# Optimization experiments

Measured on AMD Instinct MI355X. Metric: run time of the kernel, lower is better.

Reference implementation:

```python
import jax, jax.numpy as jnp
import numpy as np

KS = 3
PAD = 1
N = KS * KS  # 9 sampling taps


def conv2d(x, w, b=None):
    out = jax.lax.conv_general_dilated(
        x, w, window_strides=(1, 1), padding=((PAD, PAD), (PAD, PAD)),
        dimension_numbers=('NCHW', 'OIHW', 'NCHW'))
    if b is not None:
        out = out + b[None, :, None, None]
    return out


def deform_conv(x, w_p, b_p, w_m, b_m, w_c):
    """Modulated deformable conv (DCNv2, pure-python reference style)."""
    b, c, h, w = x.shape
    offset = conv2d(x, w_p, b_p)               # [b, 2N, h, w]
    m = jax.nn.sigmoid(conv2d(x, w_m, b_m))    # [b, N, h, w]
    xp = jnp.pad(x, ((0, 0), (0, 0), (PAD, PAD), (PAD, PAD)))
    hp, wp = h + 2 * PAD, w + 2 * PAD
    # kernel-relative offsets p_n and base grid p_0 (coords in padded image)
    r = jnp.arange(-(KS - 1) // 2, (KS - 1) // 2 + 1, dtype=x.dtype)
    pn_x, pn_y = jnp.meshgrid(r, r, indexing='ij')
    pn = jnp.concatenate([pn_x.reshape(-1), pn_y.reshape(-1)])  # [2N]
    p0_x, p0_y = jnp.meshgrid(jnp.arange(1, h + 1, dtype=x.dtype),
                              jnp.arange(1, w + 1, dtype=x.dtype), indexing='ij')
    p0 = jnp.concatenate([jnp.tile(p0_x[None], (N, 1, 1)),
                          jnp.tile(p0_y[None], (N, 1, 1))])     # [2N, h, w]
    p = jnp.transpose(offset + p0[None] + pn[None, :, None, None], (0, 2, 3, 1))  # [b,h,w,2N]
    px, py = p[..., :N], p[..., N:]
    fx, fy = jnp.floor(px), jnp.floor(py)
    q_lt_x = jnp.clip(fx, 0, hp - 1)
    q_lt_y = jnp.clip(fy, 0, wp - 1)
    q_rb_x = jnp.clip(fx + 1, 0, hp - 1)
    q_rb_y = jnp.clip(fy + 1, 0, wp - 1)
    px = jnp.clip(px, 0, hp - 1)
    py = jnp.clip(py, 0, wp - 1)
    # bilinear weights for the 4 integer corners
    g_lt = (1 + (q_lt_x - px)) * (1 + (q_lt_y - py))
    g_rb = (1 - (q_rb_x - px)) * (1 - (q_rb_y - py))
    g_lb = (1 + (q_lt_x - px)) * (1 - (q_rb_y - py))
    g_rt = (1 - (q_rb_x - px)) * (1 + (q_lt_y - py))
    xf = xp.reshape(b, c, hp * wp)

    def gather(qx, qy):
        idx = (qx * wp + qy).astype(jnp.int32).reshape(b, 1, h * w * N)
        idx = jnp.broadcast_to(idx, (b, c, h * w * N))
        return jnp.take_along_axis(xf, idx, axis=2).reshape(b, c, h, w, N)

    x_off = (g_lt[:, None] * gather(q_lt_x, q_lt_y)
             + g_rb[:, None] * gather(q_rb_x, q_rb_y)
             + g_lb[:, None] * gather(q_lt_x, q_rb_y)
             + g_rt[:, None] * gather(q_rb_x, q_lt_y))   # [b,c,h,w,N]
    x_off = x_off * jnp.transpose(m, (0, 2, 3, 1))[:, None]  # modulation
    # Conv2d(kernel=ks, stride=ks) over the reshaped taps == einsum over (c, n)
    return jnp.einsum('bchwn,ocn->bohw', x_off, w_c.reshape(w_c.shape[0], c, N))


def setup_inputs() -> dict:
    key = jax.random.key(0)
    ks = jax.random.split(key, 12)
    b, dim, hid, H, W = 8, 256, 1024, 28, 28
    inp = {
        'x': jax.random.normal(ks[0], (b, dim, H, W), jnp.float32),
        'w_p1': jax.random.normal(ks[1], (2 * N, dim, KS, KS), jnp.float32) * 0.01,
        'b_p1': jnp.zeros((2 * N,), jnp.float32),
        'w_m1': jax.random.normal(ks[2], (N, dim, KS, KS), jnp.float32) * 0.05,
        'b_m1': jnp.zeros((N,), jnp.float32),
        'w_c1': jax.random.normal(ks[3], (hid, dim, KS, KS), jnp.float32) * 0.02,
        'w_p2': jax.random.normal(ks[4], (2 * N, hid, KS, KS), jnp.float32) * 0.01,
        'b_p2': jnp.zeros((2 * N,), jnp.float32),
        'w_m2': jax.random.normal(ks[5], (N, hid, KS, KS), jnp.float32) * 0.05,
        'b_m2': jnp.zeros((N,), jnp.float32),
        'w_c2': jax.random.normal(ks[6], (dim, hid, KS, KS), jnp.float32) * 0.01,
    }
    return inp


def reference(x, w_p1, b_p1, w_m1, b_m1, w_c1, w_p2, b_p2, w_m2, b_m2, w_c2):
    h = jax.nn.relu(deform_conv(x, w_p1, b_p1, w_m1, b_m1, w_c1))
    # dropout p=0.0 -> identity (eval)
    return deform_conv(h, w_p2, b_p2, w_m2, b_m2, w_c2)
```

## Files before the change

### kernel.cpp

```cpp
#include <hip/hip_runtime.h>
#include <hip/hip_bf16.h>
#include <math.h>

#define B 8
#define HH 28
#define WDIM 28
#define PIX 784
#define PPIX 900
#define M_TOT 6272
#define NK 9
#define C1 256
#define HID 1024
#define OUT2 256
#define K1 (C1*9)
#define NY 2560
#define KSP1 12

typedef short short8_t __attribute__((ext_vector_type(8)));
typedef unsigned short us8 __attribute__((ext_vector_type(8)));
typedef unsigned short us4 __attribute__((ext_vector_type(4)));
typedef float f32x4 __attribute__((ext_vector_type(4)));

__device__ inline float bf2f(unsigned short u){ union{unsigned i; float f;} w; w.i=((unsigned)u)<<16; return w.f; }
__device__ inline unsigned short f2bf(float f){ union{float ff; unsigned i;} w; w.ff=f; unsigned u=w.i; return (unsigned short)((u + 0x7FFFu + ((u>>16)&1u))>>16); }

__device__ inline void gload16(const void* g, void* l) {
  __builtin_amdgcn_global_load_lds((const __attribute__((address_space(1))) void*)g,
                                   (__attribute__((address_space(3))) void*)l, 16, 0, 0);
}

__device__ inline int xcd_swz(int bid, int nwg) {
  int q = nwg >> 3, r = nwg & 7;
  int xcd = bid & 7, idx = bid >> 3;
  int base = (xcd < r) ? xcd * (q + 1) : r * (q + 1) + (xcd - r) * q;
  return base + idx;
}

__global__ __launch_bounds__(256) void ring_zero2(
    unsigned short* __restrict__ xclp, unsigned short* __restrict__ Y)
{
  int bid = blockIdx.x;
  unsigned short* buf; int C;
  if (bid < B * 116) { buf = xclp; C = C1; }
  else               { buf = Y; C = NY; bid -= B * 116; }
  int r = bid % 116, b = bid / 116;
  int h, w;
  if (r < 30)      { h = 0;  w = r; }
  else if (r < 60) { h = 29; w = r - 30; }
  else if (r < 88) { h = r - 59; w = 0; }
  else             { h = r - 87; w = 29; }
  unsigned short* row = buf + ((size_t)b * PPIX + h * 30 + w) * C;
  for (int c = threadIdx.x * 8; c < C; c += 2048)
    *(us8*)(row + c) = us8{0,0,0,0,0,0,0,0};
}

__global__ __launch_bounds__(256) void xpose_kernel(
    const float* __restrict__ x, unsigned short* __restrict__ xclp, int C)
{
  __shared__ unsigned short tile[32][33];
  int b = blockIdx.z, c0 = blockIdx.y * 32, p0 = blockIdx.x * 32;
  int tx = threadIdx.x & 31, ty = threadIdx.x >> 5;
  for (int i = ty; i < 32; i += 8) {
    int c = c0 + i, p = p0 + tx;
    unsigned short v = 0;
    if (p < PIX) v = f2bf(x[((size_t)b * C + c) * PIX + p]);
    tile[i][tx] = v;
  }
  __syncthreads();
  for (int i = ty; i < 32; i += 8) {
    int p = p0 + i, c = c0 + tx;
    if (p < PIX) {
      int h = p / WDIM, w = p % WDIM;
      xclp[((size_t)b * PPIX + (h + 1) * 30 + (w + 1)) * C + c] = tile[tx][i];
    }
  }
}

__global__ __launch_bounds__(256) void wprep_all(
    const float* __restrict__ wc1, const float* __restrict__ wp1,
    const float* __restrict__ wm1, const float* __restrict__ wc2,
    const float* __restrict__ wp2, const float* __restrict__ wm2,
    unsigned short* __restrict__ wr1, unsigned short* __restrict__ wpr1,
    unsigned short* __restrict__ wy2)
{
  __shared__ float lds[HID * 9];
  int bid = blockIdx.x;
  if (bid < HID) {
    for (int i = threadIdx.x; i < K1; i += 256) lds[i] = wc1[(size_t)bid * K1 + i];
    __syncthreads();
    for (int k = threadIdx.x; k < K1; k += 256) {
      int n = k >> 8, c = k & 255;
      wr1[(size_t)bid * K1 + k] = f2bf(lds[c * 9 + n]);
    }
    return;
  }
  if (bid < HID + 32) {
    int ch = bid - HID;
    const float* src = nullptr;
    if (ch < 18) src = wp1 + (size_t)ch * K1;
    else if (ch < 27) src = wm1 + (size_t)(ch - 18) * K1;
    for (int i = threadIdx.x; i < K1; i += 256) lds[i] = src ? src[i] : 0.f;
    __syncthreads();
    for (int k = threadIdx.x; k < K1; k += 256) {
      int n = k >> 8, c = k & 255;
      wpr1[(size_t)ch * K1 + k] = f2bf(lds[c * 9 + n]);
    }
    return;
  }
  bid -= HID + 32;
  if (bid >= 283) {
    int j = 2547 + (bid - 283);
    for (int c = threadIdx.x; c < HID; c += 256) wy2[(size_t)j * HID + c] = 0;
    return;
  }
  const float* src;
  if (bid < 256) src = wc2 + (size_t)bid * HID * 9;
  else {
    int ch = bid - 256;
    src = (ch < 18) ? wp2 + (size_t)ch * HID * 9 : wm2 + (size_t)(ch - 18) * HID * 9;
  }
  for (int i = threadIdx.x; i < HID * 9; i += 256) lds[i] = src[i];
  __syncthreads();
  #pragma unroll
  for (int n = 0; n < 9; ++n) {
    int j = (bid < 256) ? n * 256 + bid : 2304 + n * 27 + (bid - 256);
    for (int c = threadIdx.x; c < HID; c += 256)
      wy2[(size_t)j * HID + c] = f2bf(lds[c * 9 + n]);
  }
}

template<int C, int KSPLIT>
__global__ __launch_bounds__(256) void pconv_mfma(
    const unsigned short* __restrict__ xclp,
    const unsigned short* __restrict__ wpr,
    float* __restrict__ pmpart)
{
  __shared__ unsigned short As[2][128 * 64];
  __shared__ unsigned short Ws[2][32 * 64];
  const int K = 9 * C;
  int t = threadIdx.x, lane = t & 63, wv = t >> 6;
  int m0 = blockIdx.x * 128;
  int kz = blockIdx.y;
  int wm = (wv & 1) * 64, wo = (wv >> 1) * 16;
  f32x4 acc[4];
  #pragma unroll
  for (int i = 0; i < 4; ++i) acc[i] = {0.f, 0.f, 0.f, 0.f};
  long pbase[4];
  #pragma unroll
  for (int i = 0; i < 4; ++i) {
    int L = i * 256 + t, row = L >> 3;
    int m = m0 + row, b = m / PIX, pix = m - b * PIX;
    int h = pix / WDIM, w = pix - h * WDIM;
    pbase[i] = ((long)b * PPIX + (h + 1) * 30 + (w + 1)) * C;
  }
  auto stage = [&](int buf, int kk) {
    int n = kk / C, c0 = kk - n * C;
    long doff = (long)(((n / 3) - 1) * 30 + (n % 3) - 1) * C + c0;
    #pragma unroll
    for (int i = 0; i < 4; ++i) {
      int L = i * 256 + t, row = L >> 3, ch = L & 7;
      const char* src = (const char*)(xclp + pbase[i] + doff) + ((ch ^ (row & 7)) << 4);
      gload16(src, (char*)As[buf] + (size_t)(i * 256 + (wv << 6)) * 16);
    }
    {
      int row = t >> 3, ch = t & 7;
      const char* src = (const char*)(wpr + (size_t)row * K + kk) + ((ch ^ (row & 7)) << 4);
      gload16(src, (char*)Ws[buf] + (size_t)(wv << 6) * 16);
    }
  };

  int kbeg = kz * (K / KSPLIT), kend = kbeg + K / KSPLIT;
  stage(0, kbeg);
  asm volatile("s_waitcnt vmcnt(0)" ::: "memory");
  __syncthreads();
  int cur = 0;
  for (int k0 = kbeg; k0 < kend; k0 += 64, cur ^= 1) {
    if (k0 + 64 < kend) stage(cur ^ 1, k0 + 64);
    #pragma unroll
    for (int ks = 0; ks < 2; ++ks) {
      short8_t af[4], bq;
      {
        int row = wo + (lane & 15), ch = ks * 4 + (lane >> 4);
        bq = *(const short8_t*)((const char*)Ws[cur] + row * 128 + ((ch ^ (row & 7)) << 4));
      }
      #pragma unroll
      for (int fm = 0; fm < 4; ++fm) {
        int row = wm + fm * 16 + (lane & 15), ch = ks * 4 + (lane >> 4);
        af[fm] = *(const short8_t*)((const char*)As[cur] + row * 128 + ((ch ^ (row & 7)) << 4));
      }
      #pragma unroll
      for (int fm = 0; fm < 4; ++fm)
        acc[fm] = __builtin_amdgcn_mfma_f32_16x16x32_bf16(af[fm], bq, acc[fm], 0, 0, 0);
    }
    asm volatile("s_waitcnt vmcnt(0)" ::: "memory");
    __syncthreads();
  }
  float* dst = pmpart + (size_t)kz * M_TOT * 32;
  #pragma unroll
  for (int fm = 0; fm < 4; ++fm)
    #pragma unroll
    for (int r = 0; r < 4; ++r) {
      int ml = m0 + wm + fm * 16 + (lane >> 4) * 4 + r;
      int o = wo + (lane & 15);
      dst[(size_t)ml * 32 + o] = acc[fm][r];
    }
}

__device__ inline void mktab_emit(int m, int n, float ox, float oy, float om,
                                  const float* b_p, const float* b_m,
                                  int4* tabOff, float4* tabG)
{
  int bidx = m / PIX, pix = m % PIX;
  int hh = pix / WDIM, ww = pix % WDIM;
  float px = ox + b_p[n]     + (float)(hh + 1) + (float)(n / 3 - 1);
  float py = oy + b_p[9 + n] + (float)(ww + 1) + (float)(n % 3 - 1);
  float msk = 1.f / (1.f + expf(-(om + b_m[n])));
  float fx = floorf(px), fy = floorf(py);
  float qlx = fminf(fmaxf(fx, 0.f), 29.f);
  float qly = fminf(fmaxf(fy, 0.f), 29.f);
  float qrx = fminf(fmaxf(fx + 1.f, 0.f), 29.f);
  float qry = fminf(fmaxf(fy + 1.f, 0.f), 29.f);
  float pxc = fminf(fmaxf(px, 0.f), 29.f);
  float pyc = fminf(fmaxf(py, 0.f), 29.f);
  float glt = (1.f + (qlx - pxc)) * (1.f + (qly - pyc));
  float grb = (1.f - (qrx - pxc)) * (1.f - (qry - pyc));
  float glb = (1.f + (qlx - pxc)) * (1.f - (qry - pyc));
  float grt = (1.f - (qrx - pxc)) * (1.f + (qly - pyc));
  int ax = (int)qlx, ay = (int)qly, bx = (int)qrx, by = (int)qry;
  int pb = bidx * PPIX;
  *tabOff = make_int4(pb + ax * 30 + ay, pb + bx * 30 + by,
                      pb + ax * 30 + by, pb + bx * 30 + ay);
  *tabG   = make_float4(glt * msk, grb * msk, glb * msk, grt * msk);
}

template<int CIN, int KSPLIT>
__global__ __launch_bounds__(256) void sample_tab_kernel(
    const unsigned short* __restrict__ xclp,
    const float* __restrict__ pmpart,
    const float* __restrict__ b_p, const float* __restrict__ b_m,
    unsigned short* __restrict__ A)
{
  constexpr int LPM = CIN / 8;
  constexpr int MPB = 256 / LPM;
  __shared__ int4   stabO[MPB][NK];
  __shared__ float4 stabG[MPB][NK];
  int m0 = blockIdx.x * MPB;
  int t = threadIdx.x;
  if (t < MPB * NK) {
    int ml = t / NK, n = t % NK;
    int m = m0 + ml;
    float ox = 0.f, oy = 0.f, om = 0.f;
    #pragma unroll
    for (int kz = 0; kz < KSPLIT; ++kz) {
      const float* q = pmpart + (size_t)kz * M_TOT * 32 + (size_t)m * 32;
      ox += q[n]; oy += q[9 + n]; om += q[18 + n];
    }
    mktab_emit(m, n, ox, oy, om, b_p, b_m, &stabO[ml][n], &stabG[ml][n]);
  }
  __syncthreads();
  int mi = t / LPM;
  int c0 = (t % LPM) * 8;
  int m = m0 + mi;
  (void)m;
  unsigned short* Arow = A + (size_t)(m0 + mi) * (NK * CIN);
  #pragma unroll
  for (int n = 0; n < NK; ++n) {
    int4 o = stabO[mi][n]; float4 g = stabG[mi][n];
    us8 a0 = *(const us8*)(xclp + (size_t)o.x * CIN + c0);
    us8 a1 = *(const us8*)(xclp + (size_t)o.y * CIN + c0);
    us8 a2 = *(const us8*)(xclp + (size_t)o.z * CIN + c0);
    us8 a3 = *(const us8*)(xclp + (size_t)o.w * CIN + c0);
    us8 r;
    #pragma unroll
    for (int j = 0; j < 8; ++j) {
      float v = g.x * bf2f(a0[j]) + g.y * bf2f(a1[j])
              + g.z * bf2f(a2[j]) + g.w * bf2f(a3[j]);
      r[j] = f2bf(v);
    }
    *(us8*)(Arow + n * CIN + c0) = r;
  }
}

template<int TN, int VAR>
__global__ __launch_bounds__(256) void gemm_mfma(
    const unsigned short* __restrict__ A,
    const unsigned short* __restrict__ Wr,
    void* __restrict__ outv,
    int K, int O, int nOt, int nwg)
{
  __shared__ unsigned short As[2][128 * 64];
  __shared__ unsigned short Ws[2][TN * 64];
  constexpr int NFO = TN / 32;
  int t = threadIdx.x, lane = t & 63, wv = t >> 6;
  int swz = xcd_swz(blockIdx.x, nwg);
  int m0 = (swz / nOt) * 128, o0 = (swz % nOt) * TN;
  int wm = (wv & 1) * 64, wo = (wv >> 1) * (TN / 2);
  f32x4 acc[4][NFO];
  #pragma unroll
  for (int i = 0; i < 4; ++i)
    #pragma unroll
    for (int j = 0; j < NFO; ++j)
      acc[i][j] = {0.f, 0.f, 0.f, 0.f};

  auto stage = [&](int buf, int kk) {
    #pragma unroll
    for (int i = 0; i < 4; ++i) {
      int L = i * 256 + t, row = L >> 3, ch = L & 7;
      const char* src = (const char*)(A + (size_t)(m0 + row) * K + kk) + ((ch ^ (row & 7)) << 4);
      gload16(src, (char*)As[buf] + (size_t)(i * 256 + (wv << 6)) * 16);
    }
    #pragma unroll
    for (int i = 0; i < TN / 32; ++i) {
      int L = i * 256 + t, row = L >> 3, ch = L & 7;
      const char* src = (const char*)(Wr + (size_t)(o0 + row) * K + kk) + ((ch ^ (row & 7)) << 4);
      gload16(src, (char*)Ws[buf] + (size_t)(i * 256 + (wv << 6)) * 16);
    }
  };

  stage(0, 0);
  asm volatile("s_waitcnt vmcnt(0)" ::: "memory");
  __syncthreads();
  int cur = 0;
  for (int k0 = 0; k0 < K; k0 += 64, cur ^= 1) {
    if (k0 + 64 < K) stage(cur ^ 1, k0 + 64);
    #pragma unroll
    for (int ks = 0; ks < 2; ++ks) {
      short8_t af[4], bq[NFO];
      #pragma unroll
      for (int fm = 0; fm < 4; ++fm) {
        int row = wm + fm * 16 + (lane & 15), ch = ks * 4 + (lane >> 4);
        af[fm] = *(const short8_t*)((const char*)As[cur] + row * 128 + ((ch ^ (row & 7)) << 4));
      }
      #pragma unroll
      for (int fo = 0; fo < NFO; ++fo) {
        int row = wo + fo * 16 + (lane & 15), ch = ks * 4 + (lane >> 4);
        bq[fo] = *(const short8_t*)((const char*)Ws[cur] + row * 128 + ((ch ^ (row & 7)) << 4));
      }
      #pragma unroll
      for (int fm = 0; fm < 4; ++fm)
        #pragma unroll
        for (int fo = 0; fo < NFO; ++fo)
          acc[fm][fo] = __builtin_amdgcn_mfma_f32_16x16x32_bf16(af[fm], bq[fo], acc[fm][fo], 0, 0, 0);
    }
    asm volatile("s_waitcnt vmcnt(0)" ::: "memory");
    __syncthreads();
  }

  unsigned short* outp = (unsigned short*)outv;
  #pragma unroll
  for (int fm = 0; fm < 4; ++fm)
    #pragma unroll
    for (int r = 0; r < 4; ++r) {
      int m = m0 + wm + fm * 16 + (lane >> 4) * 4 + r;
      size_t base;
      if (VAR == 0) base = (size_t)m * O;
      else {
        int b = m / PIX, pix = m - b * PIX;
        int h = pix / WDIM, w = pix - h * WDIM;
        base = ((size_t)b * PPIX + (h + 1) * 30 + (w + 1)) * (size_t)O;
      }
      #pragma unroll
      for (int fo = 0; fo < NFO; ++fo) {
        int o = o0 + wo + fo * 16 + (lane & 15);
        float v = acc[fm][fo][r];
        if (VAR == 0) v = fmaxf(v, 0.f);
        outp[base + o] = f2bf(v);
      }
    }
}

__global__ __launch_bounds__(256) void depi2_kernel(
    const unsigned short* __restrict__ Y,
    const float* __restrict__ b_p, const float* __restrict__ b_m,
    float* __restrict__ out)
{
  __shared__ int4   stabO[4][NK];
  __shared__ float4 stabG[4][NK];
  __shared__ float tile[256][4];
  int m0 = blockIdx.x * 4;
  int t = threadIdx.x;
  if (t < 4 * NK) {
    int g = t / NK, n = t % NK;
    int m = m0 + g;
    int b = m / PIX, pix = m % PIX;
    int h = pix / WDIM, w = pix % WDIM;
    int q0 = b * PPIX + (h + 1) * 30 + (w + 1);
    float ox = 0.f, oy = 0.f, om = 0.f;
    #pragma unroll
    for (int tap = 0; tap < NK; ++tap) {
      int q = q0 + (tap / 3 - 1) * 30 + (tap % 3 - 1);
      const unsigned short* base = Y + (size_t)q * NY + 2304 + tap * 27;
      ox += bf2f(base[n]); oy += bf2f(base[9 + n]); om += bf2f(base[18 + n]);
    }
    mktab_emit(m, n, ox, oy, om, b_p, b_m, &stabO[g][n], &stabG[g][n]);
  }
  __syncthreads();
  int b = m0 / PIX, pix0 = m0 % PIX;
  int g = t >> 6, lane = t & 63;
  f32x4 acc = {0.f, 0.f, 0.f, 0.f};
  #pragma unroll
  for (int n = 0; n < NK; ++n) {
    int4 o4 = stabO[g][n]; float4 g4 = stabG[g][n];
    int col = n * 256 + lane * 4;
    us4 y0 = *(const us4*)(Y + (size_t)o4.x * NY + col);
    us4 y1 = *(const us4*)(Y + (size_t)o4.y * NY + col);
    us4 y2 = *(const us4*)(Y + (size_t)o4.z * NY + col);
    us4 y3 = *(const us4*)(Y + (size_t)o4.w * NY + col);
    #pragma unroll
    for (int j = 0; j < 4; ++j)
      acc[j] += g4.x * bf2f(y0[j]) + g4.y * bf2f(y1[j])
              + g4.z * bf2f(y2[j]) + g4.w * bf2f(y3[j]);
  }
  #pragma unroll
  for (int j = 0; j < 4; ++j) tile[lane * 4 + j][g] = acc[j];
  __syncthreads();
  int o = t;
  float4 v = *(const float4*)&tile[o][0];
  *(float4*)&out[((size_t)b * OUT2 + o) * PIX + pix0] = v;
}

extern "C" void kernel_launch(void* const* d_in, const int* in_sizes, int n_in,
                              void* d_out, int out_size, void* d_ws, size_t ws_size,
                              hipStream_t stream)
{
  const float* x    = (const float*)d_in[0];
  const float* w_p1 = (const float*)d_in[1];
  const float* b_p1 = (const float*)d_in[2];
  const float* w_m1 = (const float*)d_in[3];
  const float* b_m1 = (const float*)d_in[4];
  const float* w_c1 = (const float*)d_in[5];
  const float* w_p2 = (const float*)d_in[6];
  const float* b_p2 = (const float*)d_in[7];
  const float* w_m2 = (const float*)d_in[8];
  const float* b_m2 = (const float*)d_in[9];
  const float* w_c2 = (const float*)d_in[10];
  float* out = (float*)d_out;

  char* ws = (char*)d_ws;
  auto align_up = [](size_t v) { return (v + 255) & ~(size_t)255; };
  size_t off = 0;
  unsigned short* xclp = (unsigned short*)(ws + off); off += align_up((size_t)B * PPIX * C1 * 2);
  unsigned short* hcl  = (unsigned short*)(ws + off); off += align_up((size_t)M_TOT * HID * 2);
  unsigned short* Y    = (unsigned short*)(ws + off); off += align_up((size_t)B * PPIX * NY * 2);
  float* pmpart = (float*)(ws + off); off += align_up((size_t)KSP1 * M_TOT * 32 * 4);
  unsigned short* wr1  = (unsigned short*)(ws + off); off += align_up((size_t)HID * K1 * 2);
  unsigned short* wy2  = (unsigned short*)(ws + off); off += align_up((size_t)NY * HID * 2);
  unsigned short* wpr1 = (unsigned short*)(ws + off); off += align_up((size_t)32 * K1 * 2);
  unsigned short* Abuf = (unsigned short*)(ws + off); off += align_up((size_t)M_TOT * K1 * 2);

  ring_zero2<<<2 * B * 116, 256, 0, stream>>>(xclp, Y);
  xpose_kernel<<<dim3(25, C1 / 32, B), 256, 0, stream>>>(x, xclp, C1);
  wprep_all<<<HID + 32 + 296, 256, 0, stream>>>(
      w_c1, w_p1, w_m1, w_c2, w_p2, w_m2, wr1, wpr1, wy2);

  pconv_mfma<C1, KSP1><<<dim3(M_TOT / 128, KSP1), 256, 0, stream>>>(xclp, wpr1, pmpart);
  sample_tab_kernel<C1, KSP1><<<M_TOT / 8, 256, 0, stream>>>(
      xclp, pmpart, b_p1, b_m1, Abuf);
  {
    int nwg = (M_TOT / 128) * (HID / 128);
    gemm_mfma<128, 0><<<nwg, 256, 0, stream>>>(Abuf, wr1, hcl, K1, HID, HID / 128, nwg);
  }

  {
    int nwg = (M_TOT / 128) * (NY / 128);
    gemm_mfma<128, 3><<<nwg, 256, 0, stream>>>(hcl, wy2, Y, HID, NY, NY / 128, nwg);
  }
  depi2_kernel<<<M_TOT / 4, 256, 0, stream>>>(Y, b_p2, b_m2, out);
}
```

Measured before the change: 131.7 us.

## Merge prep kernels into one launch and deepen GEMM prefetch with partial vmcnt waits

The ring-zeroing, input-transpose and weight-prep kernels are folded into one launch with block-range dispatch, removing two kernel launches. The MFMA GEMM main loop is restructured to issue loads two stages ahead. It waits with a partial vmcnt so the next tile's loads stay in flight during compute, and raises wave priority around the MFMA block. The risk is that the partial-wait literal assumes exactly 8 loads per stage (guarded by a static_assert), and the merged prep kernel reserves the large LDS array for every block, which may limit occupancy for the small ring/transpose blocks.

```diff
diff --git a/kernel.cpp b/kernel.cpp
--- a/kernel.cpp
+++ b/kernel.cpp
@@ -36,55 +36,56 @@
   return base + idx;
 }
 
-__global__ __launch_bounds__(256) void ring_zero2(
-    unsigned short* __restrict__ xclp, unsigned short* __restrict__ Y)
-{
-  int bid = blockIdx.x;
-  unsigned short* buf; int C;
-  if (bid < B * 116) { buf = xclp; C = C1; }
-  else               { buf = Y; C = NY; bid -= B * 116; }
-  int r = bid % 116, b = bid / 116;
-  int h, w;
-  if (r < 30)      { h = 0;  w = r; }
-  else if (r < 60) { h = 29; w = r - 30; }
-  else if (r < 88) { h = r - 59; w = 0; }
-  else             { h = r - 87; w = 29; }
-  unsigned short* row = buf + ((size_t)b * PPIX + h * 30 + w) * C;
-  for (int c = threadIdx.x * 8; c < C; c += 2048)
-    *(us8*)(row + c) = us8{0,0,0,0,0,0,0,0};
-}
-
-__global__ __launch_bounds__(256) void xpose_kernel(
-    const float* __restrict__ x, unsigned short* __restrict__ xclp, int C)
-{
-  __shared__ unsigned short tile[32][33];
-  int b = blockIdx.z, c0 = blockIdx.y * 32, p0 = blockIdx.x * 32;
-  int tx = threadIdx.x & 31, ty = threadIdx.x >> 5;
-  for (int i = ty; i < 32; i += 8) {
-    int c = c0 + i, p = p0 + tx;
-    unsigned short v = 0;
-    if (p < PIX) v = f2bf(x[((size_t)b * C + c) * PIX + p]);
-    tile[i][tx] = v;
-  }
-  __syncthreads();
-  for (int i = ty; i < 32; i += 8) {
-    int p = p0 + i, c = c0 + tx;
-    if (p < PIX) {
-      int h = p / WDIM, w = p % WDIM;
-      xclp[((size_t)b * PPIX + (h + 1) * 30 + (w + 1)) * C + c] = tile[tx][i];
-    }
-  }
-}
-
-__global__ __launch_bounds__(256) void wprep_all(
+#define NRING (2 * B * 116)
+#define NXPOSE (25 * 8 * B)
+__global__ __launch_bounds__(256) void prep_all(
+    const float* __restrict__ x,
     const float* __restrict__ wc1, const float* __restrict__ wp1,
     const float* __restrict__ wm1, const float* __restrict__ wc2,
     const float* __restrict__ wp2, const float* __restrict__ wm2,
+    unsigned short* __restrict__ xclp, unsigned short* __restrict__ Y,
     unsigned short* __restrict__ wr1, unsigned short* __restrict__ wpr1,
     unsigned short* __restrict__ wy2)
 {
   __shared__ float lds[HID * 9];
   int bid = blockIdx.x;
+  if (bid < NRING) {
+    unsigned short* buf; int C;
+    if (bid < B * 116) { buf = xclp; C = C1; }
+    else               { buf = Y; C = NY; bid -= B * 116; }
+    int r = bid % 116, b = bid / 116;
+    int h, w;
+    if (r < 30)      { h = 0;  w = r; }
+    else if (r < 60) { h = 29; w = r - 30; }
+    else if (r < 88) { h = r - 59; w = 0; }
+    else             { h = r - 87; w = 29; }
+    unsigned short* row = buf + ((size_t)b * PPIX + h * 30 + w) * C;
+    for (int c = threadIdx.x * 8; c < C; c += 2048)
+      *(us8*)(row + c) = us8{0,0,0,0,0,0,0,0};
+    return;
+  }
+  bid -= NRING;
+  if (bid < NXPOSE) {
+    unsigned short (*tile)[33] = (unsigned short (*)[33])lds;
+    int p0 = (bid % 25) * 32, c0 = ((bid / 25) % 8) * 32, b = bid / 200;
+    int tx = threadIdx.x & 31, ty = threadIdx.x >> 5;
+    for (int i = ty; i < 32; i += 8) {
+      int c = c0 + i, p = p0 + tx;
+      unsigned short v = 0;
+      if (p < PIX) v = f2bf(x[((size_t)b * C1 + c) * PIX + p]);
+      tile[i][tx] = v;
+    }
+    __syncthreads();
+    for (int i = ty; i < 32; i += 8) {
+      int p = p0 + i, c = c0 + tx;
+      if (p < PIX) {
+        int h = p / WDIM, w = p % WDIM;
+        xclp[((size_t)b * PPIX + (h + 1) * 30 + (w + 1)) * C1 + c] = tile[tx][i];
+      }
+    }
+    return;
+  }
+  bid -= NXPOSE;
   if (bid < HID) {
     for (int i = threadIdx.x; i < K1; i += 256) lds[i] = wc1[(size_t)bid * K1 + i];
     __syncthreads();
@@ -260,8 +261,6 @@
   __syncthreads();
   int mi = t / LPM;
   int c0 = (t % LPM) * 8;
-  int m = m0 + mi;
-  (void)m;
   unsigned short* Arow = A + (size_t)(m0 + mi) * (NK * CIN);
   #pragma unroll
   for (int n = 0; n < NK; ++n) {
@@ -317,12 +316,15 @@
     }
   };
 
+  static_assert(TN == 128, "vmcnt literal assumes 8 loads/stage");
+  int NT = K >> 6;
   stage(0, 0);
-  asm volatile("s_waitcnt vmcnt(0)" ::: "memory");
-  __syncthreads();
-  int cur = 0;
-  for (int k0 = 0; k0 < K; k0 += 64, cur ^= 1) {
-    if (k0 + 64 < K) stage(cur ^ 1, k0 + 64);
+  stage(1, 64);
+  for (int tt = 0; tt < NT; ++tt) {
+    if (tt + 1 < NT) { asm volatile("s_waitcnt vmcnt(8)" ::: "memory"); }
+    else             { asm volatile("s_waitcnt vmcnt(0)" ::: "memory"); }
+    __builtin_amdgcn_s_barrier();
+    int cur = tt & 1;
     #pragma unroll
     for (int ks = 0; ks < 2; ++ks) {
       short8_t af[4], bq[NFO];
@@ -336,14 +338,16 @@
         int row = wo + fo * 16 + (lane & 15), ch = ks * 4 + (lane >> 4);
         bq[fo] = *(const short8_t*)((const char*)Ws[cur] + row * 128 + ((ch ^ (row & 7)) << 4));
       }
+      __builtin_amdgcn_s_setprio(1);
       #pragma unroll
       for (int fm = 0; fm < 4; ++fm)
         #pragma unroll
         for (int fo = 0; fo < NFO; ++fo)
           acc[fm][fo] = __builtin_amdgcn_mfma_f32_16x16x32_bf16(af[fm], bq[fo], acc[fm][fo], 0, 0, 0);
-    }
-    asm volatile("s_waitcnt vmcnt(0)" ::: "memory");
-    __syncthreads();
+      __builtin_amdgcn_s_setprio(0);
+    }
+    __builtin_amdgcn_s_barrier();
+    if (tt + 2 < NT) stage(cur, (tt + 2) << 6);
   }
 
   unsigned short* outp = (unsigned short*)outv;
@@ -448,10 +452,8 @@
   unsigned short* wpr1 = (unsigned short*)(ws + off); off += align_up((size_t)32 * K1 * 2);
   unsigned short* Abuf = (unsigned short*)(ws + off); off += align_up((size_t)M_TOT * K1 * 2);
 
-  ring_zero2<<<2 * B * 116, 256, 0, stream>>>(xclp, Y);
-  xpose_kernel<<<dim3(25, C1 / 32, B), 256, 0, stream>>>(x, xclp, C1);
-  wprep_all<<<HID + 32 + 296, 256, 0, stream>>>(
-      w_c1, w_p1, w_m1, w_c2, w_p2, w_m2, wr1, wpr1, wy2);
+  prep_all<<<NRING + NXPOSE + HID + 32 + 296, 256, 0, stream>>>(
+      x, w_c1, w_p1, w_m1, w_c2, w_p2, w_m2, xclp, Y, wr1, wpr1, wy2);
 
   pconv_mfma<C1, KSP1><<<dim3(M_TOT / 128, KSP1), 256, 0, stream>>>(xclp, wpr1, pmpart);
   sample_tab_kernel<C1, KSP1><<<M_TOT / 8, 256, 0, stream>>>(
```

After: 133.4 us. About the same (+1.3%).
